# Kernel tuning notes

Hardware: AMD Instinct MI355X
Metric: run time of the kernel (lower is better)

The kernel has to match this reference:

```python
import jax, jax.numpy as jnp
import numpy as np

B, NV, NC, D, E = 16, 8192, 4096, 128, 49152


def _gru_cell(x, h, w_ih, w_hh, b_ih, b_hh):
    """torch.nn.GRUCell math; gate order r, z, n; weights are (3D, D)."""
    gi = x @ w_ih.T + b_ih
    gh = h @ w_hh.T + b_hh
    ir, iz, inn = jnp.split(gi, 3, axis=-1)
    hr, hz, hn = jnp.split(gh, 3, axis=-1)
    r = jax.nn.sigmoid(ir + hr)
    z = jax.nn.sigmoid(iz + hz)
    n = jnp.tanh(inn + r * hn)
    return (1.0 - z) * n + z * h


def _msg_net(x, w1, b1, w2, b2):
    # Linear -> exact GELU -> Linear (torch nn.GELU default is erf-based)
    return jax.nn.gelu(x @ w1.T + b1, approximate=False) @ w2.T + b2


def _spmm(feats, src_idx, dst_idx, n_out):
    """Binary sparse-matrix @ dense: gather rows at src_idx, segment-sum to dst_idx.
    feats: (B, N_src, D) -> (B, n_out, D). Equivalent to torch.sparse.mm(H, feats[i])."""
    gathered = feats[:, src_idx, :]  # (B, E, D)
    return jax.vmap(lambda g: jax.ops.segment_sum(g, dst_idx, num_segments=n_out))(gathered)


def setup_inputs() -> dict:
    key = jax.random.key(0)
    ks = jax.random.split(key, 20)
    s = 0.05
    inp = {
        "v_feats": jax.random.normal(ks[0], (B, NV, D), jnp.float32),
        "c_feats": jax.random.normal(ks[1], (B, NC, D), jnp.float32),
        "edge_chk": jax.random.randint(ks[2], (E,), 0, NC, jnp.int32),
        "edge_var": jax.random.randint(ks[3], (E,), 0, NV, jnp.int32),
        # msg_net: Linear(D,D) -> GELU -> Linear(D,D)
        "msg_w1": jax.random.normal(ks[4], (D, D), jnp.float32) * s,
        "msg_b1": jnp.zeros((D,), jnp.float32),
        "msg_w2": jax.random.normal(ks[5], (D, D), jnp.float32) * s,
        "msg_b2": jnp.zeros((D,), jnp.float32),
        # var_update GRUCell(D, D)
        "var_w_ih": jax.random.normal(ks[6], (3 * D, D), jnp.float32) * s,
        "var_w_hh": jax.random.normal(ks[7], (3 * D, D), jnp.float32) * s,
        "var_b_ih": jnp.zeros((3 * D,), jnp.float32),
        "var_b_hh": jnp.zeros((3 * D,), jnp.float32),
        # chk_update GRUCell(D, D)
        "chk_w_ih": jax.random.normal(ks[8], (3 * D, D), jnp.float32) * s,
        "chk_w_hh": jax.random.normal(ks[9], (3 * D, D), jnp.float32) * s,
        "chk_b_ih": jnp.zeros((3 * D,), jnp.float32),
        "chk_b_hh": jnp.zeros((3 * D,), jnp.float32),
    }
    return inp


def reference(v_feats, c_feats, edge_chk, edge_var,
              msg_w1, msg_b1, msg_w2, msg_b2,
              var_w_ih, var_w_hh, var_b_ih, var_b_hh,
              chk_w_ih, chk_w_hh, chk_b_ih, chk_b_hh):
    b, nv, d = v_feats.shape
    nc = c_feats.shape[1]
    # variable -> check: H @ v_feats (H is binary, rows=checks, cols=vars)
    v_to_c = _spmm(v_feats, edge_var, edge_chk, nc)        # (B, NC, D)
    v_to_c = _msg_net(v_to_c, msg_w1, msg_b1, msg_w2, msg_b2)
    c_new = _gru_cell(v_to_c.reshape(-1, d), c_feats.reshape(-1, d),
                      chk_w_ih, chk_w_hh, chk_b_ih, chk_b_hh).reshape(b, nc, d)
    # check -> variable: H^T @ c_new
    c_to_v = _spmm(c_new, edge_chk, edge_var, nv)          # (B, NV, D)
    c_to_v = _msg_net(c_to_v, msg_w1, msg_b1, msg_w2, msg_b2)
    v_new = _gru_cell(c_to_v.reshape(-1, d), v_feats.reshape(-1, d),
                      var_w_ih, var_w_hh, var_b_ih, var_b_hh).reshape(b, nv, d)
    return (v_new, c_new)
```

## Files before the change

kernel.cpp:

```cpp
#include <hip/hip_runtime.h>

using u16 = unsigned short;
using u32 = unsigned int;
using u64 = unsigned long long;
typedef short short8 __attribute__((ext_vector_type(8)));
typedef unsigned short ushort8 __attribute__((ext_vector_type(8)));
typedef float f32x4 __attribute__((ext_vector_type(4)));

#define GB  16
#define GNV 8192
#define GNC 4096
#define GD  128
#define GE  49152

#define MFMA __builtin_amdgcn_mfma_f32_16x16x32_bf16
#define SB0() __builtin_amdgcn_sched_barrier(0)


__device__ __forceinline__ u16 f2bf(float f){
    u32 u = __builtin_bit_cast(u32, f);
    u32 r = (u >> 16) & 1u;
    u += 0x7fffu + r;
    return (u16)(u >> 16);
}

__device__ __forceinline__ float bf2f(u16 x){
    return __builtin_bit_cast(float, (u32)x << 16);
}

__device__ __forceinline__ u32 cvtpk(float lo, float hi){
    u32 r;
    asm("v_cvt_pk_bf16_f32 %0, %1, %2" : "=v"(r) : "v"(lo), "v"(hi));
    return r;
}

__device__ __forceinline__ ushort8 pack8(float4 v0, float4 v1){
    union { u32 u[4]; ushort8 v; } q;
    q.u[0] = cvtpk(v0.x, v0.y); q.u[1] = cvtpk(v0.z, v0.w);
    q.u[2] = cvtpk(v1.x, v1.y); q.u[3] = cvtpk(v1.z, v1.w);
    return q.v;
}

__device__ __forceinline__ u64 pack4(float a, float b, float c, float d){
    return (u64)cvtpk(a, b) | ((u64)cvtpk(c, d) << 32);
}

__device__ __forceinline__ float sigmoidf_(float x){
    return __fdividef(1.f, 1.f + __expf(-x));
}

__device__ __forceinline__ float tanhf_fast(float x){
    float xc = fminf(15.f, fmaxf(-15.f, x));
    float t  = __expf(2.f * xc);
    return __fdividef(t - 1.f, t + 1.f);
}

__device__ __forceinline__ size_t fidx(int r, int c){
    return ((size_t)(r >> 4) << 11) + ((c >> 5) << 9)
         + (((r & 15) + (((c & 31) >> 3) << 4)) << 3) + (c & 7);
}

__device__ __forceinline__ char* swzp(const void* base, int row, int bc){
    return (char*)base + row * 256 + (bc ^ ((row & 7) << 4));
}

__device__ __forceinline__ short8 ldfrag(const u16* tile, int row, int lane, int ks){
    int bc = ks * 64 + ((lane >> 4) << 4);
    return *(const short8*)swzp(tile, row, bc);
}


__global__ void k_hist(const int* __restrict__ ec, const int* __restrict__ ev,
                       int* cc, int* cv){
    int e = blockIdx.x * 256 + threadIdx.x;
    if (e < GE){ atomicAdd(&cc[ec[e]], 1); atomicAdd(&cv[ev[e]], 1); }
}

__global__ __launch_bounds__(1024) void k_scan2(const int* __restrict__ cnt_c, int* off_c, int* cur_c,
                                                const int* __restrict__ cnt_v, int* off_v, int* cur_v){
    const int* cnt = blockIdx.x ? cnt_v : cnt_c;
    int* off = blockIdx.x ? off_v : off_c;
    int* cur = blockIdx.x ? cur_v : cur_c;
    const int n = blockIdx.x ? GNV : GNC;
    __shared__ int part[1024];
    int tid = threadIdx.x;
    int chunk = n >> 10;
    int base = tid * chunk;
    int s = 0;
    for (int i = 0; i < chunk; ++i) s += cnt[base + i];
    part[tid] = s;
    __syncthreads();
    #pragma unroll
    for (int ofs = 1; ofs < 1024; ofs <<= 1){
        int v = (tid >= ofs) ? part[tid - ofs] : 0;
        __syncthreads();
        part[tid] += v;
        __syncthreads();
    }
    if (tid == 1023) off[n] = part[1023];
    int run = part[tid] - s;
    for (int i = 0; i < chunk; ++i){
        off[base + i] = run; cur[base + i] = run; run += cnt[base + i];
    }
}

__global__ void k_fill(const int* __restrict__ ec, const int* __restrict__ ev,
                       int* cur_c, int* lst_c, int* cur_v, int* lst_v){
    int e = blockIdx.x * 256 + threadIdx.x;
    if (e < GE){
        int c = ec[e], v = ev[e];
        lst_c[atomicAdd(&cur_c[c], 1)] = v;
        lst_v[atomicAdd(&cur_v[v], 1)] = c;
    }
}

__global__ void k_sort2(const int* __restrict__ off_c, int* lst_c,
                        const int* __restrict__ off_v, int* lst_v){
    int i = blockIdx.x * 256 + threadIdx.x;
    const int* off; int* lst; int idx;
    if (i < GNC){ off = off_c; lst = lst_c; idx = i; }
    else if (i < GNC + GNV){ off = off_v; lst = lst_v; idx = i - GNC; }
    else return;
    int s = off[idx], e = off[idx + 1];
    for (int a = s + 1; a < e; ++a){
        int v = lst[a]; int b = a - 1;
        while (b >= s && lst[b] > v){ lst[b + 1] = lst[b]; --b; }
        lst[b + 1] = v;
    }
}

__global__ void k_cvt6(const float* __restrict__ s0, const float* __restrict__ s1,
                       const float* __restrict__ s2, const float* __restrict__ s3,
                       const float* __restrict__ s4, const float* __restrict__ s5,
                       u16* __restrict__ dst){
    int i = blockIdx.x * 256 + threadIdx.x;
    const float* s; int off;
    if (i < 16384)       { s = s0; off = i; }
    else if (i < 32768)  { s = s1; off = i - 16384; }
    else if (i < 81920)  { s = s2; off = i - 32768; }
    else if (i < 131072) { s = s3; off = i - 81920; }
    else if (i < 180224) { s = s4; off = i - 131072; }
    else                 { s = s5; off = i - 180224; }
    dst[i] = f2bf(s[off]);
}


__global__ __launch_bounds__(256) void k_trg(const float* __restrict__ vfe,
                                             const float* __restrict__ cfe,
                                             u16* __restrict__ vT, u16* __restrict__ vF,
                                             u16* __restrict__ cF){
    const int t = threadIdx.x;
    const int ks = t >> 6, sub = (t >> 4) & 3, row = t & 15;
    const int c = ks * 32 + sub * 8;
    int gg = blockIdx.x;
    const float* src; u16* dstF; int n, b, node0, grp; u16* dstT = nullptr;
    if (gg < 8192){ b = gg >> 9; node0 = (gg & 511) << 4; grp = gg;
                    src = vfe; dstF = vF; n = GNV; dstT = vT; }
    else { int idx = gg - 8192; b = idx >> 8; node0 = (idx & 255) << 4; grp = idx;
           src = cfe; dstF = cF; n = GNC; }
    const float4* s = (const float4*)(src + ((size_t)b * n + node0 + row) * GD + c);
    float4 v0 = s[0], v1 = s[1];
    ushort8 pk = pack8(v0, v1);
    *(ushort8*)(dstF + ((size_t)grp << 11) + t * 8) = pk;
    if (dstT)
        *(ushort8*)(dstT + ((size_t)(node0 + row) << 11) + b * 128 + c) = pk;
}


__global__ __launch_bounds__(256) void k_spmm(const u16* __restrict__ srcT,
                                              const int* __restrict__ off,
                                              const int* __restrict__ lst,
                                              u16* __restrict__ dstF, int ndst){
    const int node = blockIdx.x, t = threadIdx.x;
    const int b = t >> 4, d0 = (t & 15) * 8;
    float a0[8], a1[8], a2[8], a3[8];
    #pragma unroll
    for (int i = 0; i < 8; ++i){ a0[i] = 0.f; a1[i] = 0.f; a2[i] = 0.f; a3[i] = 0.f; }
    const int s = off[node], e = off[node + 1];
    const u16* base = srcT + t * 8;
    int a = s;
    for (; a + 4 <= e; a += 4){
        ushort8 v0 = *(const ushort8*)(base + ((size_t)lst[a    ] << 11));
        ushort8 v1 = *(const ushort8*)(base + ((size_t)lst[a + 1] << 11));
        ushort8 v2 = *(const ushort8*)(base + ((size_t)lst[a + 2] << 11));
        ushort8 v3 = *(const ushort8*)(base + ((size_t)lst[a + 3] << 11));
        #pragma unroll
        for (int i = 0; i < 8; ++i){
            a0[i] += bf2f(v0[i]); a1[i] += bf2f(v1[i]);
            a2[i] += bf2f(v2[i]); a3[i] += bf2f(v3[i]);
        }
    }
    for (; a < e; ++a){
        ushort8 v = *(const ushort8*)(base + ((size_t)lst[a] << 11));
        #pragma unroll
        for (int i = 0; i < 8; ++i) a0[i] += bf2f(v[i]);
    }
    float acc[8];
    #pragma unroll
    for (int i = 0; i < 8; ++i) acc[i] = (a0[i] + a1[i]) + (a2[i] + a3[i]);
    u64* p = (u64*)(dstF + fidx(b * ndst + node, d0));
    p[0] = pack4(acc[0], acc[1], acc[2], acc[3]);
    p[1] = pack4(acc[4], acc[5], acc[6], acc[7]);
}


__global__ __launch_bounds__(256) void k_spmm_f32(const float* __restrict__ src,
                                                  const int* __restrict__ off,
                                                  const int* __restrict__ lst,
                                                  u16* __restrict__ dstF,
                                                  int ndst, int nsrc){
    const int node = blockIdx.x, t = threadIdx.x;
    const int b = t >> 4, d0 = (t & 15) * 8;
    float a0[8], a1[8], a2[8], a3[8];
    #pragma unroll
    for (int i = 0; i < 8; ++i){ a0[i] = 0.f; a1[i] = 0.f; a2[i] = 0.f; a3[i] = 0.f; }
    const int s = off[node], e = off[node + 1];
    const float* base = src + (size_t)b * nsrc * GD + d0;
    int a = s;
    for (; a + 4 <= e; a += 4){
        const float4* p0 = (const float4*)(base + ((size_t)lst[a    ] << 7));
        const float4* p1 = (const float4*)(base + ((size_t)lst[a + 1] << 7));
        const float4* p2 = (const float4*)(base + ((size_t)lst[a + 2] << 7));
        const float4* p3 = (const float4*)(base + ((size_t)lst[a + 3] << 7));
        float4 x0 = p0[0], y0 = p0[1], x1 = p1[0], y1 = p1[1];
        float4 x2 = p2[0], y2 = p2[1], x3 = p3[0], y3 = p3[1];
        a0[0]+=x0.x; a0[1]+=x0.y; a0[2]+=x0.z; a0[3]+=x0.w;
        a0[4]+=y0.x; a0[5]+=y0.y; a0[6]+=y0.z; a0[7]+=y0.w;
        a1[0]+=x1.x; a1[1]+=x1.y; a1[2]+=x1.z; a1[3]+=x1.w;
        a1[4]+=y1.x; a1[5]+=y1.y; a1[6]+=y1.z; a1[7]+=y1.w;
        a2[0]+=x2.x; a2[1]+=x2.y; a2[2]+=x2.z; a2[3]+=x2.w;
        a2[4]+=y2.x; a2[5]+=y2.y; a2[6]+=y2.z; a2[7]+=y2.w;
        a3[0]+=x3.x; a3[1]+=x3.y; a3[2]+=x3.z; a3[3]+=x3.w;
        a3[4]+=y3.x; a3[5]+=y3.y; a3[6]+=y3.z; a3[7]+=y3.w;
    }
    for (; a < e; ++a){
        const float4* p = (const float4*)(base + ((size_t)lst[a] << 7));
        float4 x = p[0], y = p[1];
        a0[0]+=x.x; a0[1]+=x.y; a0[2]+=x.z; a0[3]+=x.w;
        a0[4]+=y.x; a0[5]+=y.y; a0[6]+=y.z; a0[7]+=y.w;
    }
    float acc[8];
    #pragma unroll
    for (int i = 0; i < 8; ++i) acc[i] = (a0[i] + a1[i]) + (a2[i] + a3[i]);
    u64* p = (u64*)(dstF + fidx(b * ndst + node, d0));
    p[0] = pack4(acc[0], acc[1], acc[2], acc[3]);
    p[1] = pack4(acc[4], acc[5], acc[6], acc[7]);
}


__global__ __launch_bounds__(512) void k_msg(u16* __restrict__ X,
                                             const u16* __restrict__ W1, const float* __restrict__ b1,
                                             const u16* __restrict__ W2, const float* __restrict__ b2,
                                             int ngroups){
    __shared__ __align__(16) u16 Gs[2][16 * 128];
    const int tid = threadIdx.x, lane = tid & 63, w = tid >> 6;
    const int l15 = lane & 15, rg = lane >> 4;
    const int j = w * 16 + l15;

    short8 w1f[4], w2f[4];
    #pragma unroll
    for (int ks = 0; ks < 4; ++ks){
        w1f[ks] = *(const short8*)(W1 + (size_t)j * 128 + ks * 32 + rg * 8);
        w2f[ks] = *(const short8*)(W2 + (size_t)j * 128 + ks * 32 + rg * 8);
    }
    const float bb1 = b1[j], bb2 = b2[j];

    const int stride = gridDim.x;
    const int ng = ngroups / stride;

    short8 xA[4], xB[4];
    auto loadx = [&](short8* xf, int g){
        const u16* xb = X + ((size_t)g << 11);
        #pragma unroll
        for (int ks = 0; ks < 4; ++ks) xf[ks] = *(const short8*)(xb + ks * 512 + lane * 8);
    };
    auto g1 = [&](const short8* xf, int buf){
        f32x4 acc = {0, 0, 0, 0};
        #pragma unroll
        for (int ks = 0; ks < 4; ++ks) acc = MFMA(xf[ks], w1f[ks], acc, 0, 0, 0);
        #pragma unroll
        for (int i = 0; i < 4; ++i){
            float v = acc[i] + bb1;
            float g = 0.5f * v * (1.f + erff(v * 0.70710678f));
            *(u16*)swzp(Gs[buf], rg * 4 + i, j * 2) = f2bf(g);
        }
    };
    auto g2 = [&](int buf, int g){
        f32x4 acc = {0, 0, 0, 0};
        #pragma unroll
        for (int ks = 0; ks < 4; ++ks)
            acc = MFMA(ldfrag(Gs[buf], l15, lane, ks), w2f[ks], acc, 0, 0, 0);
        #pragma unroll
        for (int i = 0; i < 4; ++i)
            X[fidx(g * 16 + rg * 4 + i, j)] = f2bf(acc[i] + bb2);
    };

    int g = blockIdx.x;
    loadx(xA, g);
    g1(xA, 0);
    for (int k = 0; k < ng; k += 2){
        loadx(xB, g + stride);
        __syncthreads();
        g2(0, g);
        g1(xB, 1);
        if (k + 2 < ng) loadx(xA, g + 2 * stride);
        __syncthreads();
        g2(1, g + stride);
        if (k + 2 < ng) g1(xA, 0);
        g += 2 * stride;
    }
}


__global__ __launch_bounds__(512) void k_gru(const u16* __restrict__ XF, const u16* __restrict__ HF,
                                             const u16* __restrict__ Wih, const float* __restrict__ bih,
                                             const u16* __restrict__ Whh, const float* __restrict__ bhh,
                                             float* __restrict__ Out, int ngroups){
    const int tid = threadIdx.x, lane = tid & 63, w = tid >> 6;
    const int l15 = lane & 15, rg = lane >> 4;
    const int j = w * 16 + l15;

    short8 wf[6][4];
    #pragma unroll
    for (int g = 0; g < 3; ++g){
        #pragma unroll
        for (int ks = 0; ks < 4; ++ks){
            wf[g][ks]     = *(const short8*)(Wih + (size_t)(g * 128 + j) * 128 + ks * 32 + rg * 8);
            wf[g + 3][ks] = *(const short8*)(Whh + (size_t)(g * 128 + j) * 128 + ks * 32 + rg * 8);
        }
    }
    const float bir = bih[j]       + bhh[j];
    const float biz = bih[128 + j] + bhh[128 + j];
    const float bin = bih[256 + j];
    const float bhn = bhh[256 + j];

    const int h0off = ((j >> 5) << 9) + (((j & 31) >> 3) << 7) + ((rg * 4) << 3) + (j & 7);

    const int stride = gridDim.x;
    const int ng = ngroups / stride;

    short8 xfA[4], hfA[4], xfB[4], hfB[4];
    float h0A[4], h0B[4];

    auto load = [&](short8* xf, short8* hf, float* h0, int g){
        const u16* xb = XF + ((size_t)g << 11);
        const u16* hb = HF + ((size_t)g << 11);
        #pragma unroll
        for (int ks = 0; ks < 4; ++ks){
            xf[ks] = *(const short8*)(xb + ks * 512 + lane * 8);
            hf[ks] = *(const short8*)(hb + ks * 512 + lane * 8);
        }
        #pragma unroll
        for (int i = 0; i < 4; ++i) h0[i] = bf2f(hb[h0off + i * 8]);
    };

    auto comp = [&](const short8* xf, const short8* hf, const float* h0, int g){
        f32x4 ar = {0,0,0,0}, az = {0,0,0,0}, an = {0,0,0,0}, hn = {0,0,0,0};
        #pragma unroll
        for (int ks = 0; ks < 4; ++ks){
            ar = MFMA(xf[ks], wf[0][ks], ar, 0, 0, 0);
            az = MFMA(xf[ks], wf[1][ks], az, 0, 0, 0);
            an = MFMA(xf[ks], wf[2][ks], an, 0, 0, 0);
            ar = MFMA(hf[ks], wf[3][ks], ar, 0, 0, 0);
            az = MFMA(hf[ks], wf[4][ks], az, 0, 0, 0);
            hn = MFMA(hf[ks], wf[5][ks], hn, 0, 0, 0);
        }
        #pragma unroll
        for (int i = 0; i < 4; ++i){
            int r = g * 16 + rg * 4 + i;
            float rr = sigmoidf_(ar[i] + bir);
            float zz = sigmoidf_(az[i] + biz);
            float nn = tanhf_fast(an[i] + bin + rr * (hn[i] + bhn));
            Out[(size_t)r * GD + j] = (1.f - zz) * nn + zz * h0[i];
        }
    };

    int g = blockIdx.x;
    load(xfA, hfA, h0A, g);
    for (int k = 0; k < ng; k += 2){
        load(xfB, hfB, h0B, g + stride);
        SB0();
        comp(xfA, hfA, h0A, g);
        if (k + 2 < ng) load(xfA, hfA, h0A, g + 2 * stride);
        SB0();
        comp(xfB, hfB, h0B, g + stride);
        g += 2 * stride;
    }
}


extern "C" void kernel_launch(void* const* d_in, const int* in_sizes, int n_in,
                              void* d_out, int out_size, void* d_ws, size_t ws_size,
                              hipStream_t stream){
    const float* v_feats  = (const float*)d_in[0];
    const float* c_feats  = (const float*)d_in[1];
    const int*   edge_chk = (const int*)d_in[2];
    const int*   edge_var = (const int*)d_in[3];
    const float* msg_w1   = (const float*)d_in[4];
    const float* msg_b1   = (const float*)d_in[5];
    const float* msg_w2   = (const float*)d_in[6];
    const float* msg_b2   = (const float*)d_in[7];
    const float* var_w_ih = (const float*)d_in[8];
    const float* var_w_hh = (const float*)d_in[9];
    const float* var_b_ih = (const float*)d_in[10];
    const float* var_b_hh = (const float*)d_in[11];
    const float* chk_w_ih = (const float*)d_in[12];
    const float* chk_w_hh = (const float*)d_in[13];
    const float* chk_b_ih = (const float*)d_in[14];
    const float* chk_b_hh = (const float*)d_in[15];

    float* out_v = (float*)d_out;
    float* out_c = out_v + (size_t)GB * GNV * GD;

    char* p = (char*)d_ws;
    auto take = [&](size_t bytes) -> void* {
        void* r = (void*)p; p += (bytes + 255) & ~(size_t)255; return r;
    };
    int* cnt_c = (int*)take(GNC * 4);
    int* cnt_v = (int*)take(GNV * 4);
    int* off_c = (int*)take((GNC + 1) * 4);
    int* off_v = (int*)take((GNV + 1) * 4);
    int* cur_c = (int*)take(GNC * 4);
    int* cur_v = (int*)take(GNV * 4);
    int* lst_c = (int*)take(GE * 4);
    int* lst_v = (int*)take(GE * 4);
    u16* w1b  = (u16*)take((size_t)GD * GD * 2);
    u16* w2b  = (u16*)take((size_t)GD * GD * 2);
    u16* cihb = (u16*)take((size_t)3 * GD * GD * 2);
    u16* chhb = (u16*)take((size_t)3 * GD * GD * 2);
    u16* vihb = (u16*)take((size_t)3 * GD * GD * 2);
    u16* vhhb = (u16*)take((size_t)3 * GD * GD * 2);
    u16* mc = (u16*)take((size_t)GB * GNC * GD * 2);
    u16* mv = (u16*)take((size_t)GB * GNV * GD * 2);
    u16* vT = (u16*)take((size_t)GNV * GB * GD * 2);
    u16* vF = (u16*)take((size_t)GB * GNV * GD * 2);
    u16* cF = (u16*)take((size_t)GB * GNC * GD * 2);

    hipMemsetAsync(cnt_c, 0, (GNC + GNV) * 4, stream);
    k_hist<<<(GE + 255) / 256, 256, 0, stream>>>(edge_chk, edge_var, cnt_c, cnt_v);
    k_scan2<<<2, 1024, 0, stream>>>(cnt_c, off_c, cur_c, cnt_v, off_v, cur_v);
    k_fill<<<(GE + 255) / 256, 256, 0, stream>>>(edge_chk, edge_var, cur_c, lst_c, cur_v, lst_v);
    k_sort2<<<(GNC + GNV + 255) / 256, 256, 0, stream>>>(off_c, lst_c, off_v, lst_v);
    k_cvt6<<<896, 256, 0, stream>>>(msg_w1, msg_w2, chk_w_ih, chk_w_hh, var_w_ih, var_w_hh, w1b);
    k_trg<<<8192 + 4096, 256, 0, stream>>>(v_feats, c_feats, vT, vF, cF);

    k_spmm<<<GNC, 256, 0, stream>>>(vT, off_c, lst_c, mc, GNC);
    k_msg<<<512, 512, 0, stream>>>(mc, w1b, msg_b1, w2b, msg_b2, (GB * GNC) / 16);
    k_gru<<<1024, 512, 0, stream>>>(mc, cF, cihb, chk_b_ih, chhb, chk_b_hh,
                                    out_c, (GB * GNC) / 16);
    k_spmm_f32<<<GNV, 256, 0, stream>>>(out_c, off_v, lst_v, mv, GNV, GNC);
    k_msg<<<512, 512, 0, stream>>>(mv, w1b, msg_b1, w2b, msg_b2, (GB * GNV) / 16);
    k_gru<<<1024, 512, 0, stream>>>(mv, vF, vihb, var_b_ih, vhhb, var_b_hh,
                                    out_v, (GB * GNV) / 16);
}
```

Baseline: 389.3 us.

## Transpose check outputs to bf16 node-major layout and reuse bf16 SpMM

```diff
diff --git a/kernel.cpp b/kernel.cpp
--- a/kernel.cpp
+++ b/kernel.cpp
@@ -14,7 +14,6 @@
 #define GE  49152
 
 #define MFMA __builtin_amdgcn_mfma_f32_16x16x32_bf16
-#define SB0() __builtin_amdgcn_sched_barrier(0)
 
 
 __device__ __forceinline__ u16 f2bf(float f){
@@ -167,6 +166,15 @@
 }
 
 
+__global__ __launch_bounds__(256) void k_tr1(const float* __restrict__ src,
+                                             u16* __restrict__ dst, int n){
+    const int node = blockIdx.x, t = threadIdx.x;
+    const int b = t >> 4, d0 = (t & 15) * 8;
+    const float4* s = (const float4*)(src + ((size_t)b * n + node) * GD + d0);
+    *(ushort8*)(dst + ((size_t)node << 11) + b * 128 + d0) = pack8(s[0], s[1]);
+}
+
+
 __global__ __launch_bounds__(256) void k_spmm(const u16* __restrict__ srcT,
                                               const int* __restrict__ off,
                                               const int* __restrict__ lst,
@@ -204,50 +212,6 @@
 }
 
 
-__global__ __launch_bounds__(256) void k_spmm_f32(const float* __restrict__ src,
-                                                  const int* __restrict__ off,
-                                                  const int* __restrict__ lst,
-                                                  u16* __restrict__ dstF,
-                                                  int ndst, int nsrc){
-    const int node = blockIdx.x, t = threadIdx.x;
-    const int b = t >> 4, d0 = (t & 15) * 8;
-    float a0[8], a1[8], a2[8], a3[8];
-    #pragma unroll
-    for (int i = 0; i < 8; ++i){ a0[i] = 0.f; a1[i] = 0.f; a2[i] = 0.f; a3[i] = 0.f; }
-    const int s = off[node], e = off[node + 1];
-    const float* base = src + (size_t)b * nsrc * GD + d0;
-    int a = s;
-    for (; a + 4 <= e; a += 4){
-        const float4* p0 = (const float4*)(base + ((size_t)lst[a    ] << 7));
-        const float4* p1 = (const float4*)(base + ((size_t)lst[a + 1] << 7));
-        const float4* p2 = (const float4*)(base + ((size_t)lst[a + 2] << 7));
-        const float4* p3 = (const float4*)(base + ((size_t)lst[a + 3] << 7));
-        float4 x0 = p0[0], y0 = p0[1], x1 = p1[0], y1 = p1[1];
-        float4 x2 = p2[0], y2 = p2[1], x3 = p3[0], y3 = p3[1];
-        a0[0]+=x0.x; a0[1]+=x0.y; a0[2]+=x0.z; a0[3]+=x0.w;
-        a0[4]+=y0.x; a0[5]+=y0.y; a0[6]+=y0.z; a0[7]+=y0.w;
-        a1[0]+=x1.x; a1[1]+=x1.y; a1[2]+=x1.z; a1[3]+=x1.w;
-        a1[4]+=y1.x; a1[5]+=y1.y; a1[6]+=y1.z; a1[7]+=y1.w;
-        a2[0]+=x2.x; a2[1]+=x2.y; a2[2]+=x2.z; a2[3]+=x2.w;
-        a2[4]+=y2.x; a2[5]+=y2.y; a2[6]+=y2.z; a2[7]+=y2.w;
-        a3[0]+=x3.x; a3[1]+=x3.y; a3[2]+=x3.z; a3[3]+=x3.w;
-        a3[4]+=y3.x; a3[5]+=y3.y; a3[6]+=y3.z; a3[7]+=y3.w;
-    }
-    for (; a < e; ++a){
-        const float4* p = (const float4*)(base + ((size_t)lst[a] << 7));
-        float4 x = p[0], y = p[1];
-        a0[0]+=x.x; a0[1]+=x.y; a0[2]+=x.z; a0[3]+=x.w;
-        a0[4]+=y.x; a0[5]+=y.y; a0[6]+=y.z; a0[7]+=y.w;
-    }
-    float acc[8];
-    #pragma unroll
-    for (int i = 0; i < 8; ++i) acc[i] = (a0[i] + a1[i]) + (a2[i] + a3[i]);
-    u64* p = (u64*)(dstF + fidx(b * ndst + node, d0));
-    p[0] = pack4(acc[0], acc[1], acc[2], acc[3]);
-    p[1] = pack4(acc[4], acc[5], acc[6], acc[7]);
-}
-
-
 __global__ __launch_bounds__(512) void k_msg(u16* __restrict__ X,
                                              const u16* __restrict__ W1, const float* __restrict__ b1,
                                              const u16* __restrict__ W2, const float* __restrict__ b2,
@@ -379,10 +343,8 @@
     load(xfA, hfA, h0A, g);
     for (int k = 0; k < ng; k += 2){
         load(xfB, hfB, h0B, g + stride);
-        SB0();
         comp(xfA, hfA, h0A, g);
         if (k + 2 < ng) load(xfA, hfA, h0A, g + 2 * stride);
-        SB0();
         comp(xfB, hfB, h0B, g + stride);
         g += 2 * stride;
     }
@@ -433,6 +395,7 @@
     u16* mc = (u16*)take((size_t)GB * GNC * GD * 2);
     u16* mv = (u16*)take((size_t)GB * GNV * GD * 2);
     u16* vT = (u16*)take((size_t)GNV * GB * GD * 2);
+    u16* cT = (u16*)take((size_t)GNC * GB * GD * 2);
     u16* vF = (u16*)take((size_t)GB * GNV * GD * 2);
     u16* cF = (u16*)take((size_t)GB * GNC * GD * 2);
 
@@ -446,10 +409,11 @@
 
     k_spmm<<<GNC, 256, 0, stream>>>(vT, off_c, lst_c, mc, GNC);
     k_msg<<<512, 512, 0, stream>>>(mc, w1b, msg_b1, w2b, msg_b2, (GB * GNC) / 16);
-    k_gru<<<1024, 512, 0, stream>>>(mc, cF, cihb, chk_b_ih, chhb, chk_b_hh,
-                                    out_c, (GB * GNC) / 16);
-    k_spmm_f32<<<GNV, 256, 0, stream>>>(out_c, off_v, lst_v, mv, GNV, GNC);
+    k_gru<<<512, 512, 0, stream>>>(mc, cF, cihb, chk_b_ih, chhb, chk_b_hh,
+                                   out_c, (GB * GNC) / 16);
+    k_tr1<<<GNC, 256, 0, stream>>>(out_c, cT, GNC);
+    k_spmm<<<GNV, 256, 0, stream>>>(cT, off_v, lst_v, mv, GNV);
     k_msg<<<512, 512, 0, stream>>>(mv, w1b, msg_b1, w2b, msg_b2, (GB * GNV) / 16);
-    k_gru<<<1024, 512, 0, stream>>>(mv, vF, vihb, var_b_ih, vhhb, var_b_hh,
-                                    out_v, (GB * GNV) / 16);
-}
+    k_gru<<<512, 512, 0, stream>>>(mv, vF, vihb, var_b_ih, vhhb, var_b_hh,
+                                   out_v, (GB * GNV) / 16);
+}
```

Result: faster. 352.3 us (-9.5%).
